# Optimization experiments

Measured on AMD Instinct MI355X. Metric: run time of the kernel, lower is better.

## Reference

```python
import jax, jax.numpy as jnp
import numpy as np

N = 100000      # num_nodes
E = 1600000     # num edges (avg degree 16)
R = 400         # num_relations passed to GCNLayer (masks at R and 2R)
DIN, DH, DOUT = 128, 128, 128
EPS = 1e-5


def setup_inputs() -> dict:
    key = jax.random.key(0)
    ks = jax.random.split(key, 8)
    src = jax.random.randint(ks[0], (E,), 0, N)
    dst = jax.random.randint(ks[1], (E,), 0, N)
    rel = jax.random.randint(ks[2], (E,), 0, 2 * R + 1)  # covers orig/inverse/self-loop buckets
    edges = jnp.stack([src, rel, dst], axis=1)  # [E,3] = (head, rel, tail)

    def xinit(k, shape, fan_in):
        return jax.random.normal(k, shape, jnp.float32) * (1.0 / np.sqrt(fan_in))

    node_emb = xinit(ks[3], (N, DIN), DIN)
    # stacked relation-branch linears: [3, out, in] = (original, inverse, self_loop)
    W1 = xinit(ks[4], (3, DH, DIN), DIN)
    b1 = jnp.zeros((3, DH), jnp.float32)
    Ws1 = xinit(ks[5], (DH, DIN), DIN)
    bs1 = jnp.zeros((DH,), jnp.float32)
    g1 = jnp.ones((DH,), jnp.float32)
    be1 = jnp.zeros((DH,), jnp.float32)
    W2 = xinit(ks[6], (3, DOUT, DH), DH)
    b2 = jnp.zeros((3, DOUT), jnp.float32)
    Ws2 = xinit(ks[7], (DOUT, DH), DH)
    bs2 = jnp.zeros((DOUT,), jnp.float32)
    g2 = jnp.ones((DOUT,), jnp.float32)
    be2 = jnp.zeros((DOUT,), jnp.float32)
    return dict(edges=edges, node_emb=node_emb, W1=W1, b1=b1, Ws1=Ws1, bs1=bs1,
                g1=g1, be1=be1, W2=W2, b2=b2, Ws2=Ws2, bs2=bs2, g2=g2, be2=be2)


def _gcn_layer(x, src, dst, bucket, W, b):
    # Project node features once per relation branch (same math as projecting
    # gathered src features, but N << E so this is cheaper): Y[r] = x @ W[r].T + b[r]
    Y = jnp.einsum('nd,rod->rno', x, W) + b[:, None, :]     # [3, N, out]
    msgs = Y[bucket, src]                                   # [E, out] gather by (branch, src)
    n = x.shape[0]
    out = jax.ops.segment_sum(msgs, dst, num_segments=n)    # scatter-add to dst
    cnt = jax.ops.segment_sum(jnp.ones_like(dst, dtype=x.dtype), dst, num_segments=n)
    out = out / jnp.maximum(cnt, 1.0)[:, None]              # degree norm, clamp min=1
    return jax.nn.relu(out)


def _layer_norm(x, g, b):
    m = jnp.mean(x, axis=-1, keepdims=True)
    v = jnp.mean((x - m) ** 2, axis=-1, keepdims=True)
    return (x - m) * jax.lax.rsqrt(v + EPS) * g + b


def reference(edges, node_emb, W1, b1, Ws1, bs1, g1, be1, W2, b2, Ws2, bs2, g2, be2):
    src, rel, dst = edges[:, 0], edges[:, 1], edges[:, 2]
    # bucket: 0=original (rel<R), 1=inverse (R<=rel<2R), 2=self-loop (rel>=2R)
    bucket = (rel >= R).astype(jnp.int32) + (rel >= 2 * R).astype(jnp.int32)

    x1 = _gcn_layer(node_emb, src, dst, bucket, W1, b1)
    x1 = x1 + node_emb @ Ws1.T + bs1                # skip1
    x1 = _layer_norm(x1, g1, be1)                   # dropout: eval-mode identity

    x2 = _gcn_layer(x1, src, dst, bucket, W2, b2)
    x2 = x2 + x1 @ Ws2.T + bs2                      # skip2
    x2 = _layer_norm(x2, g2, be2)
    return x2
```

## Files before the change

kernel.cpp:

```cpp
#include <hip/hip_runtime.h>
#include <stdint.h>

typedef unsigned int uint;
typedef unsigned short ushort;

#define NNODES 100000
#define NPAD   100096
#define NEDGES 1600000
#define RCONST 400
#define CAP    64

#define NBKT   196
#define NBLK_A 512
#define EPB    3125
#define RUNCAP 64

typedef __attribute__((ext_vector_type(8))) short short8;
typedef __attribute__((ext_vector_type(4))) float f32x4;

__device__ __forceinline__ float bflo(uint u){ union{uint i;float f;}c; c.i=u<<16; return c.f; }
__device__ __forceinline__ float bfhi(uint u){ union{uint i;float f;}c; c.i=u&0xFFFF0000u; return c.f; }
__device__ __forceinline__ ushort f2bf(float f){ union{uint i;float ff;}c; c.ff=f; uint u=c.i;
    return (ushort)((u + 0x7FFFu + ((u>>16)&1u))>>16); }
__device__ __forceinline__ uint pack2(float lo, float hi){
    return (uint)f2bf(lo) | ((uint)f2bf(hi)<<16); }


__global__ __launch_bounds__(256) void binfill_kernel(const int* __restrict__ edges,
                                                      int* __restrict__ runcnt,
                                                      uint* __restrict__ binned) {
    __shared__ int pos[NBKT];
    int blk = blockIdx.x, tid = threadIdx.x;
    for (int i = tid; i < NBKT; i += 256) pos[i] = 0;
    __syncthreads();
    int start = blk * EPB;
    for (int i = tid; i < EPB; i += 256) {
        int e = start + i;
        int src = edges[e * 3];
        int rel = edges[e * 3 + 1];
        int dst = edges[e * 3 + 2];
        int bkt = (rel >= RCONST) + (rel >= 2 * RCONST);
        int b = dst >> 9, off = dst & 511;
        int p = atomicAdd(&pos[b], 1);
        if (p < RUNCAP)
            binned[((size_t)b * NBLK_A + blk) * RUNCAP + p] =
                (uint)src | ((uint)bkt << 17) | ((uint)off << 19);
    }
    __syncthreads();
    for (int i = tid; i < NBKT; i += 256)
        runcnt[blk * NBKT + i] = min(pos[i], RUNCAP);
}


__global__ __launch_bounds__(256) void scatter_kernel(const uint* __restrict__ binned,
                                                      const int* __restrict__ runcnt,
                                                      int* __restrict__ cnt,
                                                      int* __restrict__ elist) {
    __shared__ int c512[512];
    int b = blockIdx.x, tid = threadIdx.x;
    int base = b << 9;
    for (int i = tid; i < 512; i += 256) c512[i] = 0;
    __syncthreads();
    #pragma unroll
    for (int rr = 0; rr < 2; ++rr) {
        int r = tid * 2 + rr;
        int n = runcnt[r * NBKT + b];
        const uint* p = binned + ((size_t)b * NBLK_A + r) * RUNCAP;
        for (int i = 0; i < n; ++i) {
            uint e = p[i];
            int off = (int)(e >> 19);
            int q = atomicAdd(&c512[off], 1);
            if (q < CAP) elist[(size_t)(base + off) * CAP + q] = (int)(e & 0x7FFFFu);
        }
    }
    __syncthreads();
    for (int i = tid; i < 512; i += 256) {
        int node = base + i;
        if (node < NPAD) cnt[node] = min(c512[i], CAP);
    }
}


__global__ __launch_bounds__(256) void convx_kernel(const float* __restrict__ x,
                                                    uint* __restrict__ xb) {
    size_t i = (size_t)blockIdx.x * 256 + threadIdx.x;
    if (i < (size_t)NNODES * 64) {
        float2 f = *(const float2*)&x[i * 2];
        xb[i] = pack2(f.x, f.y);
    }
}

__global__ __launch_bounds__(256) void wconv_kernel(const float* __restrict__ W,
                                                    const float* __restrict__ Ws,
                                                    uint* __restrict__ Wb) {
    int i = blockIdx.x * 256 + threadIdx.x;
    if (i < 128 * 256) {
        int n = i >> 8, kp = i & 255, k = kp * 2;
        float v0, v1;
        if (k < 384) {
            int r = k >> 7, kk = k & 127;
            const float* p = W + r * 16384 + n * 128 + kk;
            v0 = p[0]; v1 = p[1];
        } else {
            const float* p = Ws + n * 128 + (k - 384);
            v0 = p[0]; v1 = p[1];
        }
        Wb[i] = pack2(v0, v1);
    }
}


__global__ __launch_bounds__(256) void gather_kernel(
    const uint* __restrict__ xb,
    const int* __restrict__ cnt,
    const int* __restrict__ elist,
    uint* __restrict__ Ab,
    float4* __restrict__ cnts) {
    int w = threadIdx.x >> 6, lane = threadIdx.x & 63;
    int node = blockIdx.x * 4 + w;
    int deg = min(cnt[node], CAP);
    float inv = 1.0f / fmaxf((float)deg, 1.0f);

    float a0l = 0.f, a0h = 0.f, a1l = 0.f, a1h = 0.f, a2l = 0.f, a2h = 0.f;
    int c0 = 0, c1 = 0, c2 = 0;

    for (int base = 0; base < deg; base += 64) {
        int m = min(64, deg - base);
        int ve = 0;
        if (lane < m) ve = elist[(size_t)node * CAP + base + lane];

        int j = 0;
        for (; j + 4 <= m; j += 4) {
            int e0 = __builtin_amdgcn_readlane(ve, j);
            int e1 = __builtin_amdgcn_readlane(ve, j + 1);
            int e2 = __builtin_amdgcn_readlane(ve, j + 2);
            int e3 = __builtin_amdgcn_readlane(ve, j + 3);
            int s0 = e0 & 0x1FFFF, k0 = e0 >> 17;
            int s1 = e1 & 0x1FFFF, k1 = e1 >> 17;
            int s2 = e2 & 0x1FFFF, k2 = e2 >> 17;
            int s3 = e3 & 0x1FFFF, k3 = e3 >> 17;
            uint u0 = xb[((size_t)s0 << 6) + lane];
            uint u1 = xb[((size_t)s1 << 6) + lane];
            uint u2 = xb[((size_t)s2 << 6) + lane];
            uint u3 = xb[((size_t)s3 << 6) + lane];

            float q00 = (k0 == 0) ? 1.f : 0.f, q01 = (k0 == 1) ? 1.f : 0.f, q02 = (k0 == 2) ? 1.f : 0.f;
            float q10 = (k1 == 0) ? 1.f : 0.f, q11 = (k1 == 1) ? 1.f : 0.f, q12 = (k1 == 2) ? 1.f : 0.f;
            float q20 = (k2 == 0) ? 1.f : 0.f, q21 = (k2 == 1) ? 1.f : 0.f, q22 = (k2 == 2) ? 1.f : 0.f;
            float q30 = (k3 == 0) ? 1.f : 0.f, q31 = (k3 == 1) ? 1.f : 0.f, q32 = (k3 == 2) ? 1.f : 0.f;
            c0 += (k0 == 0) + (k1 == 0) + (k2 == 0) + (k3 == 0);
            c1 += (k0 == 1) + (k1 == 1) + (k2 == 1) + (k3 == 1);
            c2 += (k0 == 2) + (k1 == 2) + (k2 == 2) + (k3 == 2);

            float f0l = bflo(u0), f0h = bfhi(u0);
            float f1l = bflo(u1), f1h = bfhi(u1);
            float f2l = bflo(u2), f2h = bfhi(u2);
            float f3l = bflo(u3), f3h = bfhi(u3);

            a0l = fmaf(q00, f0l, a0l); a1l = fmaf(q01, f0l, a1l); a2l = fmaf(q02, f0l, a2l);
            a0h = fmaf(q00, f0h, a0h); a1h = fmaf(q01, f0h, a1h); a2h = fmaf(q02, f0h, a2h);
            a0l = fmaf(q10, f1l, a0l); a1l = fmaf(q11, f1l, a1l); a2l = fmaf(q12, f1l, a2l);
            a0h = fmaf(q10, f1h, a0h); a1h = fmaf(q11, f1h, a1h); a2h = fmaf(q12, f1h, a2h);
            a0l = fmaf(q20, f2l, a0l); a1l = fmaf(q21, f2l, a1l); a2l = fmaf(q22, f2l, a2l);
            a0h = fmaf(q20, f2h, a0h); a1h = fmaf(q21, f2h, a1h); a2h = fmaf(q22, f2h, a2h);
            a0l = fmaf(q30, f3l, a0l); a1l = fmaf(q31, f3l, a1l); a2l = fmaf(q32, f3l, a2l);
            a0h = fmaf(q30, f3h, a0h); a1h = fmaf(q31, f3h, a1h); a2h = fmaf(q32, f3h, a2h);
        }
        for (; j < m; ++j) {
            int ee = __builtin_amdgcn_readlane(ve, j);
            int s = ee & 0x1FFFF, k = ee >> 17;
            uint u = xb[((size_t)s << 6) + lane];
            float q0 = (k == 0) ? 1.f : 0.f;
            float q1 = (k == 1) ? 1.f : 0.f;
            float q2 = (k == 2) ? 1.f : 0.f;
            c0 += (k == 0); c1 += (k == 1); c2 += (k == 2);
            float fl = bflo(u), fh = bfhi(u);
            a0l = fmaf(q0, fl, a0l); a1l = fmaf(q1, fl, a1l); a2l = fmaf(q2, fl, a2l);
            a0h = fmaf(q0, fh, a0h); a1h = fmaf(q1, fh, a1h); a2h = fmaf(q2, fh, a2h);
        }
    }

    size_t ab = (size_t)node * 192 + lane;
    Ab[ab]       = pack2(a0l * inv, a0h * inv);
    Ab[ab + 64]  = pack2(a1l * inv, a1h * inv);
    Ab[ab + 128] = pack2(a2l * inv, a2h * inv);
    if (lane == 0) {
        float4 v; v.x = (float)c0; v.y = (float)c1; v.z = (float)c2; v.w = inv;
        cnts[node] = v;
    }
}


template<bool OUT_BF16>
__global__ __launch_bounds__(256, 3) void gemm_kernel(
    const ushort* __restrict__ Ab,
    const ushort* __restrict__ xb,
    const ushort* __restrict__ Wb,
    const float* __restrict__ bia,
    const float* __restrict__ bs,
    const float* __restrict__ g,
    const float* __restrict__ be,
    const float4* __restrict__ cnts,
    void* __restrict__ out) {
    __shared__ ushort lA[64 * 64];
    __shared__ ushort lB[128 * 64];
    __shared__ float sS1[4][64], sS2[4][64];
    __shared__ float sMean[64], sRstd[64];

    int tid = threadIdx.x;
    int w = tid >> 6, lane = tid & 63;
    int wn = w;
    int quad = lane >> 4, l15 = lane & 15;
    int node0 = blockIdx.x * 64;

    int arow = tid >> 2, aseg = tid & 3;
    int brow = tid >> 1, bseg = (tid & 1) * 4;
    uint swzA = (uint)((arow & 7) << 4);
    uint swzB = (uint)((brow & 7) << 4);
    uint swzR = (uint)((l15 & 7) << 4);

    const ushort* gA = Ab + (size_t)node0 * 384;
    const ushort* gX = xb + (size_t)node0 * 128;

    f32x4 accm[4][2], accq[4][2];
    f32x4 zero = {0.f, 0.f, 0.f, 0.f};
    #pragma unroll
    for (int i = 0; i < 4; ++i)
        #pragma unroll
        for (int j = 0; j < 2; ++j) { accm[i][j] = zero; accq[i][j] = zero; }

    uint4 ra0, ra1, rb0, rb1, rb2, rb3;
    auto load_chunk = [&](int t) {
        const ushort* srcA; size_t strA;
        if (t < 6) { srcA = gA + t * 64;       strA = 384; }
        else       { srcA = gX + (t - 6) * 64; strA = 128; }
        const ushort* pa = srcA + (size_t)arow * strA + aseg * 8;
        ra0 = *(const uint4*)(pa);
        ra1 = *(const uint4*)(pa + 32);
        const ushort* pb = Wb + t * 64 + (size_t)brow * 512 + bseg * 8;
        rb0 = *(const uint4*)(pb);
        rb1 = *(const uint4*)(pb + 8);
        rb2 = *(const uint4*)(pb + 16);
        rb3 = *(const uint4*)(pb + 24);
    };
    auto compute = [&](f32x4 (&acc)[4][2]) {
        #pragma unroll
        for (int ks = 0; ks < 2; ++ks) {
            short8 aF[4], bF[2];
            #pragma unroll
            for (int mt = 0; mt < 4; ++mt) {
                int row = mt * 16 + l15;
                aF[mt] = *(const short8*)((const char*)lA + row * 128 +
                                          (((uint)(ks * 64 + quad * 16)) ^ swzR));
            }
            #pragma unroll
            for (int nt = 0; nt < 2; ++nt) {
                int row = wn * 32 + nt * 16 + l15;
                bF[nt] = *(const short8*)((const char*)lB + row * 128 +
                                          (((uint)(ks * 64 + quad * 16)) ^ swzR));
            }
            #pragma unroll
            for (int mt = 0; mt < 4; ++mt)
                #pragma unroll
                for (int nt = 0; nt < 2; ++nt)
                    acc[mt][nt] = __builtin_amdgcn_mfma_f32_16x16x32_bf16(
                        aF[mt], bF[nt], acc[mt][nt], 0, 0, 0);
        }
    };

    load_chunk(0);
    for (int t = 0; t < 8; ++t) {
        if (t) __syncthreads();
        {
            char* bA = (char*)lA + arow * 128;
            *(uint4*)(bA + (((uint)(aseg * 16)) ^ swzA))       = ra0;
            *(uint4*)(bA + (((uint)((aseg + 4) * 16)) ^ swzA)) = ra1;
            char* bB = (char*)lB + brow * 128;
            *(uint4*)(bB + (((uint)((bseg + 0) * 16)) ^ swzB)) = rb0;
            *(uint4*)(bB + (((uint)((bseg + 1) * 16)) ^ swzB)) = rb1;
            *(uint4*)(bB + (((uint)((bseg + 2) * 16)) ^ swzB)) = rb2;
            *(uint4*)(bB + (((uint)((bseg + 3) * 16)) ^ swzB)) = rb3;
        }
        __syncthreads();
        if (t < 7) load_chunk(t + 1);
        if (t < 6) compute(accm); else compute(accq);
    }

    int nl0 = wn * 32 + l15;
    float pb0[2], pb1[2], pb2[2], pbs[2], pg[2], pbe[2];
    #pragma unroll
    for (int nt = 0; nt < 2; ++nt) {
        int nl = nl0 + nt * 16;
        pb0[nt] = bia[nl]; pb1[nt] = bia[128 + nl]; pb2[nt] = bia[256 + nl];
        pbs[nt] = bs[nl];  pg[nt] = g[nl];          pbe[nt] = be[nl];
    }
    #pragma unroll
    for (int mt = 0; mt < 4; ++mt) {
        #pragma unroll
        for (int r = 0; r < 4; ++r) {
            int ml = mt * 16 + quad * 4 + r;
            float4 c4 = cnts[node0 + ml];
            float s1 = 0.f, s2 = 0.f;
            #pragma unroll
            for (int nt = 0; nt < 2; ++nt) {
                float bd = (c4.x * pb0[nt] + c4.y * pb1[nt] + c4.z * pb2[nt]) * c4.w;
                float v = fmaxf(accm[mt][nt][r] + bd, 0.f) + accq[mt][nt][r] + pbs[nt];
                accm[mt][nt][r] = v;
                s1 += v; s2 += v * v;
            }
            #pragma unroll
            for (int mask = 1; mask < 16; mask <<= 1) {
                s1 += __shfl_xor(s1, mask);
                s2 += __shfl_xor(s2, mask);
            }
            if (l15 == 0) { sS1[wn][ml] = s1; sS2[wn][ml] = s2; }
        }
    }
    __syncthreads();
    if (tid < 64) {
        float s1 = sS1[0][tid] + sS1[1][tid] + sS1[2][tid] + sS1[3][tid];
        float s2 = sS2[0][tid] + sS2[1][tid] + sS2[2][tid] + sS2[3][tid];
        float mean = s1 * (1.f / 128.f);
        float var = s2 * (1.f / 128.f) - mean * mean;
        sMean[tid] = mean;
        sRstd[tid] = rsqrtf(var + 1e-5f);
    }
    __syncthreads();
    #pragma unroll
    for (int mt = 0; mt < 4; ++mt) {
        #pragma unroll
        for (int r = 0; r < 4; ++r) {
            int ml = mt * 16 + quad * 4 + r;
            int node = node0 + ml;
            float mn = sMean[ml], rs = sRstd[ml];
            #pragma unroll
            for (int nt = 0; nt < 2; ++nt) {
                float v = (accm[mt][nt][r] - mn) * rs * pg[nt] + pbe[nt];
                if (OUT_BF16) {
                    float vh = __shfl_xor(v, 1);
                    if (!(l15 & 1) && node < NNODES) {
                        uint* o = (uint*)out;
                        o[(size_t)node * 64 + wn * 16 + nt * 8 + (l15 >> 1)] = pack2(v, vh);
                    }
                } else {
                    if (node < NNODES) {
                        float* o = (float*)out;
                        o[(size_t)node * 128 + nl0 + nt * 16] = v;
                    }
                }
            }
        }
    }
}


extern "C" void kernel_launch(void* const* d_in, const int* in_sizes, int n_in,
                              void* d_out, int out_size, void* d_ws, size_t ws_size,
                              hipStream_t stream) {
    (void)in_sizes; (void)n_in; (void)out_size; (void)ws_size;

    const int*   edges = (const int*)d_in[0];
    const float* xemb  = (const float*)d_in[1];
    const float* W1  = (const float*)d_in[2];
    const float* b1  = (const float*)d_in[3];
    const float* Ws1 = (const float*)d_in[4];
    const float* bs1 = (const float*)d_in[5];
    const float* g1  = (const float*)d_in[6];
    const float* be1 = (const float*)d_in[7];
    const float* W2  = (const float*)d_in[8];
    const float* b2  = (const float*)d_in[9];
    const float* Ws2 = (const float*)d_in[10];
    const float* bs2 = (const float*)d_in[11];
    const float* g2  = (const float*)d_in[12];
    const float* be2 = (const float*)d_in[13];

    char* ws = (char*)d_ws;
    auto take = [&](size_t bytes) {
        char* p = ws;
        ws += (bytes + 255) & ~(size_t)255;
        return p;
    };
    int*    cnt    = (int*)take((size_t)NPAD * 4);
    int*    elist  = (int*)take((size_t)NPAD * CAP * 4);
    float4* cnts   = (float4*)take((size_t)NPAD * 16);
    uint*   xb0    = (uint*)take((size_t)NPAD * 128 * 2);
    uint*   xb1    = (uint*)take((size_t)NPAD * 128 * 2);
    uint*   Ab     = (uint*)take((size_t)NPAD * 384 * 2);
    uint*   Wb1    = (uint*)take((size_t)128 * 512 * 2);
    uint*   Wb2    = (uint*)take((size_t)128 * 512 * 2);
    int*    runcnt = (int*)take((size_t)NBLK_A * NBKT * 4);
    uint*   binned = (uint*)take((size_t)NBKT * NBLK_A * RUNCAP * 4);

    binfill_kernel<<<NBLK_A, 256, 0, stream>>>(edges, runcnt, binned);
    scatter_kernel<<<NBKT, 256, 0, stream>>>(binned, runcnt, cnt, elist);

    convx_kernel<<<(NNODES * 64) / 256, 256, 0, stream>>>(xemb, xb0);
    wconv_kernel<<<128, 256, 0, stream>>>(W1, Ws1, Wb1);
    wconv_kernel<<<128, 256, 0, stream>>>(W2, Ws2, Wb2);

    gather_kernel<<<NNODES / 4, 256, 0, stream>>>(xb0, cnt, elist, Ab, cnts);
    gemm_kernel<true><<<NPAD / 64, 256, 0, stream>>>(
        (const ushort*)Ab, (const ushort*)xb0, (const ushort*)Wb1,
        b1, bs1, g1, be1, cnts, xb1);

    gather_kernel<<<NNODES / 4, 256, 0, stream>>>(xb1, cnt, elist, Ab, cnts);
    gemm_kernel<false><<<NPAD / 64, 256, 0, stream>>>(
        (const ushort*)Ab, (const ushort*)xb1, (const ushort*)Wb2,
        b2, bs2, g2, be2, cnts, d_out);
}
```

Before: 402.4 us.

## Sort edge lists by relation bucket and gather two edges per wave

The scatter pass now counts edges per destination per relation bucket, lays each node's edge list out grouped by bucket, and pads each group to an even length with a zero row. The gather kernel then needs no per-edge bucket select or masked FMAs. Each half-wave loads a different edge's row with 8-byte loads and the halves are combined with a cross-lane shuffle. Per-bucket counts and the inverse degree move into the scatter kernel. In exchange, scatter reads the binned edges twice, and the padding rows and the always-64-wide edge-list load add some extra memory traffic.

Result: slower. 421.6 us (+4.8%).

```diff
diff --git a/kernel.cpp b/kernel.cpp
--- a/kernel.cpp
+++ b/kernel.cpp
@@ -9,6 +9,7 @@
 #define NEDGES 1600000
 #define RCONST 400
 #define CAP    64
+#define ZROW   NNODES
 
 #define NBKT   196
 #define NBLK_A 512
@@ -17,6 +18,7 @@
 
 typedef __attribute__((ext_vector_type(8))) short short8;
 typedef __attribute__((ext_vector_type(4))) float f32x4;
+typedef __attribute__((ext_vector_type(2))) float f32x2;
 
 __device__ __forceinline__ float bflo(uint u){ union{uint i;float f;}c; c.i=u<<16; return c.f; }
 __device__ __forceinline__ float bfhi(uint u){ union{uint i;float f;}c; c.i=u&0xFFFF0000u; return c.f; }
@@ -54,12 +56,14 @@
 
 __global__ __launch_bounds__(256) void scatter_kernel(const uint* __restrict__ binned,
                                                       const int* __restrict__ runcnt,
-                                                      int* __restrict__ cnt,
-                                                      int* __restrict__ elist) {
-    __shared__ int c512[512];
+                                                      int* __restrict__ elist,
+                                                      uint* __restrict__ segp,
+                                                      float4* __restrict__ cnts) {
+    __shared__ int cnt3[512][4];
+    __shared__ int cur[512][4];
     int b = blockIdx.x, tid = threadIdx.x;
     int base = b << 9;
-    for (int i = tid; i < 512; i += 256) c512[i] = 0;
+    for (int i = tid; i < 512; i += 256) { cnt3[i][0] = 0; cnt3[i][1] = 0; cnt3[i][2] = 0; }
     __syncthreads();
     #pragma unroll
     for (int rr = 0; rr < 2; ++rr) {
@@ -68,15 +72,43 @@
         const uint* p = binned + ((size_t)b * NBLK_A + r) * RUNCAP;
         for (int i = 0; i < n; ++i) {
             uint e = p[i];
-            int off = (int)(e >> 19);
-            int q = atomicAdd(&c512[off], 1);
-            if (q < CAP) elist[(size_t)(base + off) * CAP + q] = (int)(e & 0x7FFFFu);
+            atomicAdd(&cnt3[e >> 19][(e >> 17) & 3], 1);
         }
     }
     __syncthreads();
     for (int i = tid; i < 512; i += 256) {
         int node = base + i;
-        if (node < NPAD) cnt[node] = min(c512[i], CAP);
+        if (node >= NPAD) continue;
+        int c0 = cnt3[i][0], c1 = cnt3[i][1], c2 = cnt3[i][2];
+        int n0 = min((c0 + 1) & ~1, 64);
+        int n1 = min((c1 + 1) & ~1, 64 - n0);
+        int n2 = min((c2 + 1) & ~1, 64 - n0 - n1);
+        int s1 = n0, s2 = n0 + n1, tot = n0 + n1 + n2;
+        cur[i][0] = 0; cur[i][1] = s1; cur[i][2] = s2;
+        int* er = elist + (size_t)node * 64;
+        for (int j = min(c0, n0); j < n0; ++j) er[j] = ZROW;
+        for (int j = min(c1, n1); j < n1; ++j) er[s1 + j] = ZROW;
+        for (int j = min(c2, n2); j < n2; ++j) er[s2 + j] = ZROW;
+        cnt3[i][0] = s1; cnt3[i][1] = s2; cnt3[i][2] = tot;
+        segp[node] = (uint)n0 | ((uint)n1 << 8) | ((uint)n2 << 16);
+        float4 v;
+        v.x = (float)c0; v.y = (float)c1; v.z = (float)c2;
+        v.w = 1.0f / fmaxf((float)(c0 + c1 + c2), 1.0f);
+        cnts[node] = v;
+    }
+    __syncthreads();
+    #pragma unroll
+    for (int rr = 0; rr < 2; ++rr) {
+        int r = tid * 2 + rr;
+        int n = runcnt[r * NBKT + b];
+        const uint* p = binned + ((size_t)b * NBLK_A + r) * RUNCAP;
+        for (int i = 0; i < n; ++i) {
+            uint e = p[i];
+            int off = (int)(e >> 19), bk = (int)((e >> 17) & 3);
+            int pos = atomicAdd(&cur[off][bk], 1);
+            if (pos < cnt3[off][bk])
+                elist[(size_t)(base + off) * 64 + pos] = (int)(e & 0x1FFFFu);
+        }
     }
 }
 
@@ -84,9 +116,13 @@
 __global__ __launch_bounds__(256) void convx_kernel(const float* __restrict__ x,
                                                     uint* __restrict__ xb) {
     size_t i = (size_t)blockIdx.x * 256 + threadIdx.x;
-    if (i < (size_t)NNODES * 64) {
-        float2 f = *(const float2*)&x[i * 2];
-        xb[i] = pack2(f.x, f.y);
+    if (i < (size_t)NPAD * 64) {
+        uint val = 0;
+        if (i < (size_t)NNODES * 64) {
+            float2 f = *(const float2*)&x[i * 2];
+            val = pack2(f.x, f.y);
+        }
+        xb[i] = val;
     }
 }
 
@@ -112,81 +148,55 @@
 
 __global__ __launch_bounds__(256) void gather_kernel(
     const uint* __restrict__ xb,
-    const int* __restrict__ cnt,
-    const int* __restrict__ elist,
-    uint* __restrict__ Ab,
-    float4* __restrict__ cnts) {
-    int w = threadIdx.x >> 6, lane = threadIdx.x & 63;
+    const uint* __restrict__ segp,
+    const int*  __restrict__ elist,
+    const float4* __restrict__ cnts,
+    uint* __restrict__ Ab) {
+    int tid = threadIdx.x;
+    int w = tid >> 6, lane = tid & 63;
     int node = blockIdx.x * 4 + w;
-    int deg = min(cnt[node], CAP);
-    float inv = 1.0f / fmaxf((float)deg, 1.0f);
-
-    float a0l = 0.f, a0h = 0.f, a1l = 0.f, a1h = 0.f, a2l = 0.f, a2h = 0.f;
-    int c0 = 0, c1 = 0, c2 = 0;
-
-    for (int base = 0; base < deg; base += 64) {
-        int m = min(64, deg - base);
-        int ve = 0;
-        if (lane < m) ve = elist[(size_t)node * CAP + base + lane];
-
-        int j = 0;
-        for (; j + 4 <= m; j += 4) {
-            int e0 = __builtin_amdgcn_readlane(ve, j);
-            int e1 = __builtin_amdgcn_readlane(ve, j + 1);
-            int e2 = __builtin_amdgcn_readlane(ve, j + 2);
-            int e3 = __builtin_amdgcn_readlane(ve, j + 3);
-            int s0 = e0 & 0x1FFFF, k0 = e0 >> 17;
-            int s1 = e1 & 0x1FFFF, k1 = e1 >> 17;
-            int s2 = e2 & 0x1FFFF, k2 = e2 >> 17;
-            int s3 = e3 & 0x1FFFF, k3 = e3 >> 17;
-            uint u0 = xb[((size_t)s0 << 6) + lane];
-            uint u1 = xb[((size_t)s1 << 6) + lane];
-            uint u2 = xb[((size_t)s2 << 6) + lane];
-            uint u3 = xb[((size_t)s3 << 6) + lane];
-
-            float q00 = (k0 == 0) ? 1.f : 0.f, q01 = (k0 == 1) ? 1.f : 0.f, q02 = (k0 == 2) ? 1.f : 0.f;
-            float q10 = (k1 == 0) ? 1.f : 0.f, q11 = (k1 == 1) ? 1.f : 0.f, q12 = (k1 == 2) ? 1.f : 0.f;
-            float q20 = (k2 == 0) ? 1.f : 0.f, q21 = (k2 == 1) ? 1.f : 0.f, q22 = (k2 == 2) ? 1.f : 0.f;
-            float q30 = (k3 == 0) ? 1.f : 0.f, q31 = (k3 == 1) ? 1.f : 0.f, q32 = (k3 == 2) ? 1.f : 0.f;
-            c0 += (k0 == 0) + (k1 == 0) + (k2 == 0) + (k3 == 0);
-            c1 += (k0 == 1) + (k1 == 1) + (k2 == 1) + (k3 == 1);
-            c2 += (k0 == 2) + (k1 == 2) + (k2 == 2) + (k3 == 2);
-
-            float f0l = bflo(u0), f0h = bfhi(u0);
-            float f1l = bflo(u1), f1h = bfhi(u1);
-            float f2l = bflo(u2), f2h = bfhi(u2);
-            float f3l = bflo(u3), f3h = bfhi(u3);
-
-            a0l = fmaf(q00, f0l, a0l); a1l = fmaf(q01, f0l, a1l); a2l = fmaf(q02, f0l, a2l);
-            a0h = fmaf(q00, f0h, a0h); a1h = fmaf(q01, f0h, a1h); a2h = fmaf(q02, f0h, a2h);
-            a0l = fmaf(q10, f1l, a0l); a1l = fmaf(q11, f1l, a1l); a2l = fmaf(q12, f1l, a2l);
-            a0h = fmaf(q10, f1h, a0h); a1h = fmaf(q11, f1h, a1h); a2h = fmaf(q12, f1h, a2h);
-            a0l = fmaf(q20, f2l, a0l); a1l = fmaf(q21, f2l, a1l); a2l = fmaf(q22, f2l, a2l);
-            a0h = fmaf(q20, f2h, a0h); a1h = fmaf(q21, f2h, a1h); a2h = fmaf(q22, f2h, a2h);
-            a0l = fmaf(q30, f3l, a0l); a1l = fmaf(q31, f3l, a1l); a2l = fmaf(q32, f3l, a2l);
-            a0h = fmaf(q30, f3h, a0h); a1h = fmaf(q31, f3h, a1h); a2h = fmaf(q32, f3h, a2h);
-        }
-        for (; j < m; ++j) {
-            int ee = __builtin_amdgcn_readlane(ve, j);
-            int s = ee & 0x1FFFF, k = ee >> 17;
-            uint u = xb[((size_t)s << 6) + lane];
-            float q0 = (k == 0) ? 1.f : 0.f;
-            float q1 = (k == 1) ? 1.f : 0.f;
-            float q2 = (k == 2) ? 1.f : 0.f;
-            c0 += (k == 0); c1 += (k == 1); c2 += (k == 2);
-            float fl = bflo(u), fh = bfhi(u);
-            a0l = fmaf(q0, fl, a0l); a1l = fmaf(q1, fl, a1l); a2l = fmaf(q2, fl, a2l);
-            a0h = fmaf(q0, fh, a0h); a1h = fmaf(q1, fh, a1h); a2h = fmaf(q2, fh, a2h);
-        }
-    }
-
-    size_t ab = (size_t)node * 192 + lane;
-    Ab[ab]       = pack2(a0l * inv, a0h * inv);
-    Ab[ab + 64]  = pack2(a1l * inv, a1h * inv);
-    Ab[ab + 128] = pack2(a2l * inv, a2h * inv);
-    if (lane == 0) {
-        float4 v; v.x = (float)c0; v.y = (float)c1; v.z = (float)c2; v.w = inv;
-        cnts[node] = v;
+    uint sp = __builtin_amdgcn_readfirstlane(segp[node]);
+    float inv = cnts[node].w;
+    int ve = elist[(size_t)node * 64 + lane];
+    int half = lane >> 5, hl = lane & 31;
+    const char* xrow = (const char*)xb + (hl << 3);
+
+    f32x2 a00 = {0.f, 0.f}, a01 = {0.f, 0.f};
+    f32x2 a10 = {0.f, 0.f}, a11 = {0.f, 0.f};
+    f32x2 a20 = {0.f, 0.f}, a21 = {0.f, 0.f};
+    int n0 = (int)(sp & 255), n1 = (int)((sp >> 8) & 255), n2 = (int)((sp >> 16) & 255);
+    int eb = 0;
+
+    #define SEG(NB, A0, A1)                                                   \
+    for (int j = 0; j < NB; j += 2) {                                         \
+        int sA = __builtin_amdgcn_readlane(ve, eb + j);                       \
+        int sB = __builtin_amdgcn_readlane(ve, eb + j + 1);                   \
+        int ss = half ? sB : sA;                                              \
+        uint2 u = *(const uint2*)(xrow + ((size_t)((uint)ss << 8)));          \
+        f32x2 f0 = {bflo(u.x), bfhi(u.x)};                                    \
+        f32x2 f1 = {bflo(u.y), bfhi(u.y)};                                    \
+        A0 += f0; A1 += f1;                                                   \
+    }                                                                         \
+    eb += NB;
+
+    SEG(n0, a00, a01)
+    SEG(n1, a10, a11)
+    SEG(n2, a20, a21)
+    #undef SEG
+
+    #define COMB(A) { f32x2 t; t.x = __shfl_xor(A.x, 32); t.y = __shfl_xor(A.y, 32); \
+                      A += t; A *= inv; }
+    COMB(a00) COMB(a01) COMB(a10) COMB(a11) COMB(a20) COMB(a21)
+    #undef COMB
+
+    if (half == 0) {
+        size_t ab = (size_t)node * 192 + hl * 2;
+        uint2 v0 = { pack2(a00.x, a00.y), pack2(a01.x, a01.y) };
+        *(uint2*)&Ab[ab] = v0;
+        uint2 v1 = { pack2(a10.x, a10.y), pack2(a11.x, a11.y) };
+        *(uint2*)&Ab[ab + 64] = v1;
+        uint2 v2 = { pack2(a20.x, a20.y), pack2(a21.x, a21.y) };
+        *(uint2*)&Ab[ab + 128] = v2;
     }
 }
 
@@ -338,9 +348,10 @@
                 float v = (accm[mt][nt][r] - mn) * rs * pg[nt] + pbe[nt];
                 if (OUT_BF16) {
                     float vh = __shfl_xor(v, 1);
-                    if (!(l15 & 1) && node < NNODES) {
+                    if (!(l15 & 1)) {
+                        uint val = (node < NNODES) ? pack2(v, vh) : 0u;
                         uint* o = (uint*)out;
-                        o[(size_t)node * 64 + wn * 16 + nt * 8 + (l15 >> 1)] = pack2(v, vh);
+                        o[(size_t)node * 64 + wn * 16 + nt * 8 + (l15 >> 1)] = val;
                     }
                 } else {
                     if (node < NNODES) {
@@ -380,8 +391,8 @@
         ws += (bytes + 255) & ~(size_t)255;
         return p;
     };
-    int*    cnt    = (int*)take((size_t)NPAD * 4);
     int*    elist  = (int*)take((size_t)NPAD * CAP * 4);
+    uint*   segp   = (uint*)take((size_t)NPAD * 4);
     float4* cnts   = (float4*)take((size_t)NPAD * 16);
     uint*   xb0    = (uint*)take((size_t)NPAD * 128 * 2);
     uint*   xb1    = (uint*)take((size_t)NPAD * 128 * 2);
@@ -392,18 +403,18 @@
     uint*   binned = (uint*)take((size_t)NBKT * NBLK_A * RUNCAP * 4);
 
     binfill_kernel<<<NBLK_A, 256, 0, stream>>>(edges, runcnt, binned);
-    scatter_kernel<<<NBKT, 256, 0, stream>>>(binned, runcnt, cnt, elist);
-
-    convx_kernel<<<(NNODES * 64) / 256, 256, 0, stream>>>(xemb, xb0);
+    scatter_kernel<<<NBKT, 256, 0, stream>>>(binned, runcnt, elist, segp, cnts);
+
+    convx_kernel<<<(NPAD * 64) / 256, 256, 0, stream>>>(xemb, xb0);
     wconv_kernel<<<128, 256, 0, stream>>>(W1, Ws1, Wb1);
     wconv_kernel<<<128, 256, 0, stream>>>(W2, Ws2, Wb2);
 
-    gather_kernel<<<NNODES / 4, 256, 0, stream>>>(xb0, cnt, elist, Ab, cnts);
+    gather_kernel<<<NNODES / 4, 256, 0, stream>>>(xb0, segp, elist, cnts, Ab);
     gemm_kernel<true><<<NPAD / 64, 256, 0, stream>>>(
         (const ushort*)Ab, (const ushort*)xb0, (const ushort*)Wb1,
         b1, bs1, g1, be1, cnts, xb1);
 
-    gather_kernel<<<NNODES / 4, 256, 0, stream>>>(xb1, cnt, elist, Ab, cnts);
+    gather_kernel<<<NNODES / 4, 256, 0, stream>>>(xb1, segp, elist, cnts, Ab);
     gemm_kernel<false><<<NPAD / 64, 256, 0, stream>>>(
         (const ushort*)Ab, (const ushort*)xb1, (const ushort*)Wb2,
         b2, bs2, g2, be2, cnts, d_out);
```
